# Kernel optimization log

Hardware: AMD Instinct MI355X
Metric: run time of the kernel (lower is better)

## Reference

```python
import jax, jax.numpy as jnp
import numpy as np

D_MODEL = 1024
N_HEAD = 16


def setup_inputs() -> dict:
    key = jax.random.key(0)
    ks = jax.random.split(key, 11)
    B, S, D = 2, 2048, D_MODEL
    scale = 1.0 / np.sqrt(D)
    inp = {
        "query_tensor": jax.random.normal(ks[0], (B, S, D), jnp.float32),
        "key_tensor": jax.random.normal(ks[1], (B, S, D), jnp.float32),
        "value_tensor": jax.random.normal(ks[2], (B, S, D), jnp.float32),
        "w_q": jax.random.normal(ks[3], (D, D), jnp.float32) * scale,
        "b_q": jnp.zeros((D,), jnp.float32),
        "w_k": jax.random.normal(ks[4], (D, D), jnp.float32) * scale,
        "b_k": jnp.zeros((D,), jnp.float32),
        "w_v": jax.random.normal(ks[5], (D, D), jnp.float32) * scale,
        "b_v": jnp.zeros((D,), jnp.float32),
        "w_out": jax.random.normal(ks[6], (D, D), jnp.float32) * scale,
        "b_out": jnp.zeros((D,), jnp.float32),
    }
    return inp


def _split_heads(x, n_head):
    b, s, d = x.shape
    return x.reshape(b, s, n_head, d // n_head).transpose(0, 2, 1, 3)  # [b,h,s,dk]


def reference(query_tensor, key_tensor, value_tensor, w_q, b_q, w_k, b_k, w_v, b_v, w_out, b_out):
    # torch Linear: y = x @ W.T + b
    q = query_tensor @ w_q.T + b_q
    k = key_tensor @ w_k.T + b_k
    v = value_tensor @ w_v.T + b_v
    q = _split_heads(q, N_HEAD)
    k = _split_heads(k, N_HEAD)
    v = _split_heads(v, N_HEAD)
    d_k = k.shape[-1]
    scores = jnp.einsum("bhqd,bhkd->bhqk", q, k) / jnp.sqrt(jnp.float32(d_k))
    attn = jax.nn.softmax(scores, axis=-1)
    ctx = jnp.einsum("bhqk,bhkd->bhqd", attn, v)
    b, h, s, dk = ctx.shape
    ctx = ctx.transpose(0, 2, 1, 3).reshape(b, s, h * dk)
    return ctx @ w_out.T + b_out
```

## Files before the change

### kernel.cpp

```cpp
#include <hip/hip_runtime.h>
#include <hip/hip_bf16.h>

using ushort = unsigned short;

typedef __attribute__((ext_vector_type(8))) short bf16x8;
typedef __attribute__((ext_vector_type(4))) float f32x4;
typedef __attribute__((ext_vector_type(16))) float f32x16;
typedef __attribute__((ext_vector_type(4))) unsigned short u16x4;

#define DEVINL __device__ __forceinline__


static constexpr size_t XQ_O = 0;
static constexpr size_t WQ_O = 12582912;
static constexpr size_t WO_O = 15728640;
static constexpr size_t QB_O = 16777216;
static constexpr size_t KB_O = 20971520;
static constexpr size_t VT_O = 25165824;
static constexpr size_t CTX_O = 0;

DEVINL ushort f2bf(float f) {
  unsigned u = __builtin_bit_cast(unsigned, f);
  u += 0x7fffu + ((u >> 16) & 1u);
  return (ushort)(u >> 16);
}

DEVINL void gld16(const ushort* g, ushort* lds) {
  __builtin_amdgcn_global_load_lds(
      (const __attribute__((address_space(1))) void*)g,
      (__attribute__((address_space(3))) void*)lds, 16, 0, 0);
}

__global__ __launch_bounds__(256) void cvt_all(
    const float* __restrict__ xq, const float* __restrict__ xk, const float* __restrict__ xv,
    const float* __restrict__ wq, const float* __restrict__ wk, const float* __restrict__ wv,
    const float* __restrict__ wo, ushort* __restrict__ ws)
{
  int e = (blockIdx.x * 256 + threadIdx.x) * 8;
  const float* s;
  if      (e < 4194304)  s = xq + e;
  else if (e < 8388608)  s = xk + (e - 4194304);
  else if (e < 12582912) s = xv + (e - 8388608);
  else if (e < 13631488) s = wq + (e - 12582912);
  else if (e < 14680064) s = wk + (e - 13631488);
  else if (e < 15728640) s = wv + (e - 14680064);
  else                   s = wo + (e - 15728640);
  float4 a = *(const float4*)s;
  float4 b = *(const float4*)(s + 4);
  union { u16x4 v; ushort u[4]; } r0, r1;
  r0.u[0] = f2bf(a.x); r0.u[1] = f2bf(a.y); r0.u[2] = f2bf(a.z); r0.u[3] = f2bf(a.w);
  r1.u[0] = f2bf(b.x); r1.u[1] = f2bf(b.y); r1.u[2] = f2bf(b.z); r1.u[3] = f2bf(b.w);
  *(u16x4*)(ws + e) = r0.v;
  *(u16x4*)(ws + e + 4) = r1.v;
}

DEVINL void gemm_core(const ushort* __restrict__ A, const ushort* __restrict__ Bw,
                      const float* __restrict__ bias, void* __restrict__ Cout,
                      float scale, int omode, int row0, int col0)
{
  constexpr int K = 1024;
  __shared__ ushort As[128 * 64];
  __shared__ ushort Bs[128 * 64];
  const int t = threadIdx.x;
  const int l = t & 63;
  const int w = t >> 6;
  const int wr = w >> 1, wc = w & 1;

  const int srow = t >> 3;
  const int scol8 = (t & 7) * 8;
  const int swz_half = ((((t & 7) * 16) ^ ((srow & 7) << 4)) >> 1);

  const ushort* Ap = A + (size_t)(row0 + srow) * K + scol8;
  const ushort* Bp = Bw + (size_t)(col0 + srow) * K + scol8;

  bf16x8 areg[4], breg[4];
  auto loadstage = [&](int k0) {
#pragma unroll
    for (int i = 0; i < 4; ++i) {
      areg[i] = *(const bf16x8*)(Ap + (size_t)(i * 32) * K + k0);
      breg[i] = *(const bf16x8*)(Bp + (size_t)(i * 32) * K + k0);
    }
  };

  f32x4 acc[4][4];
#pragma unroll
  for (int i = 0; i < 4; ++i)
#pragma unroll
    for (int j = 0; j < 4; ++j) acc[i][j] = (f32x4){0.f, 0.f, 0.f, 0.f};

  loadstage(0);
#pragma unroll 1
  for (int kt = 0; kt < K / 64; ++kt) {
    __syncthreads();
#pragma unroll
    for (int i = 0; i < 4; ++i) {
      *(bf16x8*)&As[(srow + i * 32) * 64 + swz_half] = areg[i];
      *(bf16x8*)&Bs[(srow + i * 32) * 64 + swz_half] = breg[i];
    }
    if (kt + 1 < K / 64) loadstage((kt + 1) * 64);
    __syncthreads();
#pragma unroll
    for (int ks = 0; ks < 2; ++ks) {
      bf16x8 af[4], bfr[4];
#pragma unroll
      for (int mi = 0; mi < 4; ++mi) {
        int r = wr * 64 + mi * 16 + (l & 15);
        int cb = ((ks << 6) | ((l >> 4) << 4)) ^ ((r & 7) << 4);
        af[mi] = *(const bf16x8*)&As[r * 64 + (cb >> 1)];
      }
#pragma unroll
      for (int nj = 0; nj < 4; ++nj) {
        int r = wc * 64 + nj * 16 + (l & 15);
        int cb = ((ks << 6) | ((l >> 4) << 4)) ^ ((r & 7) << 4);
        bfr[nj] = *(const bf16x8*)&Bs[r * 64 + (cb >> 1)];
      }
#pragma unroll
      for (int mi = 0; mi < 4; ++mi)
#pragma unroll
        for (int nj = 0; nj < 4; ++nj)
          acc[mi][nj] = __builtin_amdgcn_mfma_f32_16x16x32_bf16(af[mi], bfr[nj], acc[mi][nj], 0, 0, 0);
    }
  }

  const int cl = l & 15;
#pragma unroll
  for (int mi = 0; mi < 4; ++mi) {
#pragma unroll
    for (int nj = 0; nj < 4; ++nj) {
      int n = col0 + wc * 64 + nj * 16 + cl;
      float bv = bias[n];
      int mbase = row0 + wr * 64 + mi * 16 + (l >> 4) * 4;
      if (omode == 1) {
        float* Of = (float*)Cout;
#pragma unroll
        for (int ri = 0; ri < 4; ++ri)
          Of[(size_t)(mbase + ri) * 1024 + n] = (acc[mi][nj][ri] + bv) * scale;
      } else if (omode == 0) {
        ushort* Ob = (ushort*)Cout;
        int h = n >> 6, d = n & 63;
#pragma unroll
        for (int ri = 0; ri < 4; ++ri) {
          int m = mbase + ri;
          int b = m >> 11, s = m & 2047;
          Ob[(size_t)((b * 16 + h) * 2048 + s) * 64 + d] = f2bf((acc[mi][nj][ri] + bv) * scale);
        }
      } else {
        ushort* Ob = (ushort*)Cout;
        int h = n >> 6, d = n & 63;
        int b = mbase >> 11, s = mbase & 2047;
        union { u16x4 v; ushort u[4]; } pk;
#pragma unroll
        for (int ri = 0; ri < 4; ++ri) pk.u[ri] = f2bf((acc[mi][nj][ri] + bv) * scale);
        *(u16x4*)&Ob[(size_t)((b * 16 + h) * 64 + d) * 2048 + s] = pk.v;
      }
    }
  }
}

__global__ __launch_bounds__(256, 2) void gemm_qkv(
    const ushort* __restrict__ ws_c, ushort* __restrict__ ws_m,
    const float* __restrict__ bq, const float* __restrict__ bk, const float* __restrict__ bv)
{
  const int z = blockIdx.z;
  const ushort* A = ws_c + XQ_O + (size_t)z * 4194304;
  const ushort* W = ws_c + WQ_O + (size_t)z * 1048576;
  const float* bias = (z == 0) ? bq : ((z == 1) ? bk : bv);
  ushort* dst = ws_m + QB_O + (size_t)z * 4194304;
  float scale = (z == 0) ? (0.125f * 1.4426950408889634f) : 1.0f;
  int omode = (z == 2) ? 2 : 0;
  gemm_core(A, W, bias, dst, scale, omode, blockIdx.y * 128, blockIdx.x * 128);
}

__global__ __launch_bounds__(256, 2) void gemm_out(
    const ushort* __restrict__ ctx, const ushort* __restrict__ wo,
    const float* __restrict__ bo, float* __restrict__ out)
{
  gemm_core(ctx, wo, bo, out, 1.0f, 1, blockIdx.y * 128, blockIdx.x * 128);
}

__global__ __launch_bounds__(512, 4) void attn8(
    const ushort* __restrict__ Qb, const ushort* __restrict__ Kb,
    const ushort* __restrict__ Vtb, ushort* __restrict__ Ctx)
{
  __shared__ ushort smem[32768];

  const int t = threadIdx.x, l = t & 63, w = t >> 6;
  const int wq4 = w & 3, half = w >> 2;
  const int hi2 = l >> 5, q = l & 31;
  const int bh = blockIdx.y, qt = blockIdx.x;
  const int kvb = half * 1024;
  const ushort* Qp = Qb + ((size_t)bh * 2048 + qt * 128 + wq4 * 32) * 64;
  const ushort* Kp = Kb + (size_t)bh * 2048 * 64;
  const ushort* Vp = Vtb + (size_t)bh * 64 * 2048;

  ushort* Ksh = smem + half * 8192;
  ushort* Vsh = smem + 16384 + half * 8192;

  bf16x8 qf[4];
#pragma unroll
  for (int ks = 0; ks < 4; ++ks)
    qf[ks] = *(const bf16x8*)(Qp + q * 64 + ks * 16 + hi2 * 8);

  auto stageKV = [&](int pp, int kv0) {
#pragma unroll
    for (int i = 0; i < 2; ++i) {
      int R = (i * 4 + wq4) * 8 + (l >> 3);
      int g = l & 7;
      int sR = (R & ~12) | ((R & 4) << 1) | ((R & 8) >> 1);
      gld16(Kp + (size_t)(kv0 + sR) * 64 + (g ^ (R & 7)) * 8,
            Ksh + pp * 4096 + (i * 4 + wq4) * 512);
      gld16(Vp + (size_t)R * 2048 + kv0 + (g ^ (R & 7)) * 8,
            Vsh + pp * 4096 + (i * 4 + wq4) * 512);
    }
  };

  f32x16 acc0, acc1;
#pragma unroll
  for (int i = 0; i < 16; ++i) { acc0[i] = 0.f; acc1[i] = 0.f; }
  f32x16 Zv;
#pragma unroll
  for (int i = 0; i < 16; ++i) Zv[i] = 0.f;
  float lrun = 0.f;

  const int rsw = (q & 7) << 4;

  stageKV(0, kvb);
  __syncthreads();

#pragma unroll 1
  for (int kt = 0; kt < 16; ++kt) {
    const int p = kt & 1;
    const ushort* Kl = Ksh + p * 4096;
    const ushort* Vl = Vsh + p * 4096;

    f32x16 scA, scB;
    __builtin_amdgcn_s_setprio(1);
    {
      bf16x8 kf = *(const bf16x8*)&Kl[q * 64 + (((hi2 * 16)) ^ rsw) / 2];
      scA = __builtin_amdgcn_mfma_f32_32x32x16_bf16(kf, qf[0], Zv, 0, 0, 0);
#pragma unroll
      for (int ks = 1; ks < 4; ++ks) {
        bf16x8 k2 = *(const bf16x8*)&Kl[q * 64 + (((ks * 32 + hi2 * 16) ^ rsw) >> 1)];
        scA = __builtin_amdgcn_mfma_f32_32x32x16_bf16(k2, qf[ks], scA, 0, 0, 0);
      }
      const int r1 = (32 + q) * 64;
      bf16x8 kg = *(const bf16x8*)&Kl[r1 + (((hi2 * 16)) ^ rsw) / 2];
      scB = __builtin_amdgcn_mfma_f32_32x32x16_bf16(kg, qf[0], Zv, 0, 0, 0);
#pragma unroll
      for (int ks = 1; ks < 4; ++ks) {
        bf16x8 k2 = *(const bf16x8*)&Kl[r1 + (((ks * 32 + hi2 * 16) ^ rsw) >> 1)];
        scB = __builtin_amdgcn_mfma_f32_32x32x16_bf16(k2, qf[ks], scB, 0, 0, 0);
      }
    }
    __builtin_amdgcn_s_setprio(0);

    if (kt + 1 < 16) stageKV(p ^ 1, kvb + (kt + 1) * 64);

#pragma unroll
    for (int c = 0; c < 2; ++c) {
      f32x16& sc = (c == 0) ? scA : scB;
      float s0 = 0.f, s1 = 0.f, s2 = 0.f, s3 = 0.f;
#pragma unroll
      for (int i = 0; i < 4; ++i) {
        float e0 = __builtin_amdgcn_exp2f(sc[i]);      sc[i] = e0;      s0 += e0;
        float e1 = __builtin_amdgcn_exp2f(sc[4 + i]);  sc[4 + i] = e1;  s1 += e1;
        float e2 = __builtin_amdgcn_exp2f(sc[8 + i]);  sc[8 + i] = e2;  s2 += e2;
        float e3 = __builtin_amdgcn_exp2f(sc[12 + i]); sc[12 + i] = e3; s3 += e3;
      }
      lrun += (s0 + s1) + (s2 + s3);

      union PU { bf16x8 v; unsigned u[4]; } pA, pB;
#pragma unroll
      for (int i = 0; i < 4; ++i) {
        asm("v_cvt_pk_bf16_f32 %0, %1, %2" : "=v"(pA.u[i]) : "v"(sc[2 * i]), "v"(sc[2 * i + 1]));
        asm("v_cvt_pk_bf16_f32 %0, %1, %2" : "=v"(pB.u[i]) : "v"(sc[8 + 2 * i]), "v"(sc[9 + 2 * i]));
      }

      __builtin_amdgcn_s_setprio(1);
#pragma unroll
      for (int db = 0; db < 2; ++db) {
        const int d = db * 32 + q;
        bf16x8 va = *(const bf16x8*)&Vl[d * 64 + (((c * 64 + hi2 * 16) ^ rsw) >> 1)];
        bf16x8 vb = *(const bf16x8*)&Vl[d * 64 + (((c * 64 + 32 + hi2 * 16) ^ rsw) >> 1)];
        if (db == 0) {
          acc0 = __builtin_amdgcn_mfma_f32_32x32x16_bf16(va, pA.v, acc0, 0, 0, 0);
          acc0 = __builtin_amdgcn_mfma_f32_32x32x16_bf16(vb, pB.v, acc0, 0, 0, 0);
        } else {
          acc1 = __builtin_amdgcn_mfma_f32_32x32x16_bf16(va, pA.v, acc1, 0, 0, 0);
          acc1 = __builtin_amdgcn_mfma_f32_32x32x16_bf16(vb, pB.v, acc1, 0, 0, 0);
        }
      }
      __builtin_amdgcn_s_setprio(0);
    }
    __syncthreads();
  }

  float lsum = lrun + __shfl_xor(lrun, 32);
  float* Lf = (float*)smem;

  if (l < 32) Lf[half * 128 + wq4 * 32 + q] = lsum;
  __syncthreads();
  const float inv = 1.0f / (Lf[wq4 * 32 + q] + Lf[128 + wq4 * 32 + q]);
  __syncthreads();

  if (half == 1) {
    float* base = Lf + (wq4 * 32 + q) * 64;
#pragma unroll
    for (int db = 0; db < 2; ++db)
#pragma unroll
      for (int g = 0; g < 4; ++g) {
        float4 v;
        if (db == 0) v = (float4){acc0[g * 4], acc0[g * 4 + 1], acc0[g * 4 + 2], acc0[g * 4 + 3]};
        else         v = (float4){acc1[g * 4], acc1[g * 4 + 1], acc1[g * 4 + 2], acc1[g * 4 + 3]};
        *(float4*)(base + db * 32 + g * 8 + hi2 * 4) = v;
      }
  }
  __syncthreads();

  if (half == 0) {
    float* base = Lf + (wq4 * 32 + q) * 64;
#pragma unroll
    for (int db = 0; db < 2; ++db)
#pragma unroll
      for (int g = 0; g < 4; ++g) {
        float* p = base + db * 32 + g * 8 + hi2 * 4;
        float4 pv = *(float4*)p;
        float4 o;
        if (db == 0) o = (float4){(acc0[g * 4] + pv.x) * inv, (acc0[g * 4 + 1] + pv.y) * inv,
                                  (acc0[g * 4 + 2] + pv.z) * inv, (acc0[g * 4 + 3] + pv.w) * inv};
        else         o = (float4){(acc1[g * 4] + pv.x) * inv, (acc1[g * 4 + 1] + pv.y) * inv,
                                  (acc1[g * 4 + 2] + pv.z) * inv, (acc1[g * 4 + 3] + pv.w) * inv};
        *(float4*)p = o;
      }
  }
  __syncthreads();

  {
    const int b = bh >> 4, h = bh & 15;
    const int d0 = (l & 7) * 8;
#pragma unroll
    for (int rr = 0; rr < 2; ++rr) {
      int row = w * 16 + rr * 8 + (l >> 3);
      float4 f0 = *(const float4*)(Lf + row * 64 + d0);
      float4 f1 = *(const float4*)(Lf + row * 64 + d0 + 4);
      union { u16x4 v; ushort u[4]; } o0, o1;
      o0.u[0] = f2bf(f0.x); o0.u[1] = f2bf(f0.y); o0.u[2] = f2bf(f0.z); o0.u[3] = f2bf(f0.w);
      o1.u[0] = f2bf(f1.x); o1.u[1] = f2bf(f1.y); o1.u[2] = f2bf(f1.z); o1.u[3] = f2bf(f1.w);
      ushort* dst = Ctx + ((size_t)b * 2048 + qt * 128 + row) * 1024 + h * 64 + d0;
      *(u16x4*)dst = o0.v;
      *(u16x4*)(dst + 4) = o1.v;
    }
  }
}

extern "C" void kernel_launch(void* const* d_in, const int* in_sizes, int n_in,
                              void* d_out, int out_size, void* d_ws, size_t ws_size,
                              hipStream_t stream) {
  const float* xq = (const float*)d_in[0];
  const float* xk = (const float*)d_in[1];
  const float* xv = (const float*)d_in[2];
  const float* wq = (const float*)d_in[3];
  const float* bq = (const float*)d_in[4];
  const float* wk = (const float*)d_in[5];
  const float* bk = (const float*)d_in[6];
  const float* wv = (const float*)d_in[7];
  const float* bv = (const float*)d_in[8];
  const float* wo = (const float*)d_in[9];
  const float* bo = (const float*)d_in[10];
  ushort* ws = (ushort*)d_ws;

  cvt_all<<<8192, 256, 0, stream>>>(xq, xk, xv, wq, wk, wv, wo, ws);
  gemm_qkv<<<dim3(8, 32, 3), 256, 0, stream>>>(ws, ws, bq, bk, bv);
  attn8<<<dim3(16, 32), 512, 0, stream>>>(ws + QB_O, ws + KB_O, ws + VT_O, ws + CTX_O);
  gemm_out<<<dim3(8, 32), 256, 0, stream>>>(ws + CTX_O, ws + WO_O, bo, (float*)d_out);
}
```

Before: 116.9 us.

## Narrow output GEMM tile, remap attention blocks, swizzle merge LDS buffer

The output projection GEMM is templated on N-tile width and now uses 128x64 tiles, doubling its grid to 512 blocks so more CUs on the MI355X are busy. The attention kernel remaps block indices so that concurrently scheduled blocks share heads, which should improve L2 reuse of K/V. The fp32 LDS merge buffer is XOR-swizzled to cut bank conflicts during the two-half reduction and bf16 writeout. The narrower tile lowers per-block arithmetic intensity for the output GEMM.

New measurement: 114.4 us. 2.1% less time.

```diff
diff --git a/kernel.cpp b/kernel.cpp
--- a/kernel.cpp
+++ b/kernel.cpp
@@ -54,13 +54,16 @@
   *(u16x4*)(ws + e + 4) = r1.v;
 }
 
+template<int BN>
 DEVINL void gemm_core(const ushort* __restrict__ A, const ushort* __restrict__ Bw,
                       const float* __restrict__ bias, void* __restrict__ Cout,
                       float scale, int omode, int row0, int col0)
 {
   constexpr int K = 1024;
+  constexpr int BI = BN / 32;
+  constexpr int NJ = BN / 32;
   __shared__ ushort As[128 * 64];
-  __shared__ ushort Bs[128 * 64];
+  __shared__ ushort Bs[BN * 64];
   const int t = threadIdx.x;
   const int l = t & 63;
   const int w = t >> 6;
@@ -73,35 +76,37 @@
   const ushort* Ap = A + (size_t)(row0 + srow) * K + scol8;
   const ushort* Bp = Bw + (size_t)(col0 + srow) * K + scol8;
 
-  bf16x8 areg[4], breg[4];
+  bf16x8 areg[4], breg[BI];
   auto loadstage = [&](int k0) {
 #pragma unroll
-    for (int i = 0; i < 4; ++i) {
+    for (int i = 0; i < 4; ++i)
       areg[i] = *(const bf16x8*)(Ap + (size_t)(i * 32) * K + k0);
+#pragma unroll
+    for (int i = 0; i < BI; ++i)
       breg[i] = *(const bf16x8*)(Bp + (size_t)(i * 32) * K + k0);
-    }
   };
 
-  f32x4 acc[4][4];
+  f32x4 acc[4][NJ];
 #pragma unroll
   for (int i = 0; i < 4; ++i)
 #pragma unroll
-    for (int j = 0; j < 4; ++j) acc[i][j] = (f32x4){0.f, 0.f, 0.f, 0.f};
+    for (int j = 0; j < NJ; ++j) acc[i][j] = (f32x4){0.f, 0.f, 0.f, 0.f};
 
   loadstage(0);
 #pragma unroll 1
   for (int kt = 0; kt < K / 64; ++kt) {
     __syncthreads();
 #pragma unroll
-    for (int i = 0; i < 4; ++i) {
+    for (int i = 0; i < 4; ++i)
       *(bf16x8*)&As[(srow + i * 32) * 64 + swz_half] = areg[i];
+#pragma unroll
+    for (int i = 0; i < BI; ++i)
       *(bf16x8*)&Bs[(srow + i * 32) * 64 + swz_half] = breg[i];
-    }
     if (kt + 1 < K / 64) loadstage((kt + 1) * 64);
     __syncthreads();
 #pragma unroll
     for (int ks = 0; ks < 2; ++ks) {
-      bf16x8 af[4], bfr[4];
+      bf16x8 af[4], bfr[NJ];
 #pragma unroll
       for (int mi = 0; mi < 4; ++mi) {
         int r = wr * 64 + mi * 16 + (l & 15);
@@ -109,15 +114,15 @@
         af[mi] = *(const bf16x8*)&As[r * 64 + (cb >> 1)];
       }
 #pragma unroll
-      for (int nj = 0; nj < 4; ++nj) {
-        int r = wc * 64 + nj * 16 + (l & 15);
+      for (int nj = 0; nj < NJ; ++nj) {
+        int r = wc * (BN / 2) + nj * 16 + (l & 15);
         int cb = ((ks << 6) | ((l >> 4) << 4)) ^ ((r & 7) << 4);
         bfr[nj] = *(const bf16x8*)&Bs[r * 64 + (cb >> 1)];
       }
 #pragma unroll
       for (int mi = 0; mi < 4; ++mi)
 #pragma unroll
-        for (int nj = 0; nj < 4; ++nj)
+        for (int nj = 0; nj < NJ; ++nj)
           acc[mi][nj] = __builtin_amdgcn_mfma_f32_16x16x32_bf16(af[mi], bfr[nj], acc[mi][nj], 0, 0, 0);
     }
   }
@@ -126,8 +131,8 @@
 #pragma unroll
   for (int mi = 0; mi < 4; ++mi) {
 #pragma unroll
-    for (int nj = 0; nj < 4; ++nj) {
-      int n = col0 + wc * 64 + nj * 16 + cl;
+    for (int nj = 0; nj < NJ; ++nj) {
+      int n = col0 + wc * (BN / 2) + nj * 16 + cl;
       float bv = bias[n];
       int mbase = row0 + wr * 64 + mi * 16 + (l >> 4) * 4;
       if (omode == 1) {
@@ -168,14 +173,14 @@
   ushort* dst = ws_m + QB_O + (size_t)z * 4194304;
   float scale = (z == 0) ? (0.125f * 1.4426950408889634f) : 1.0f;
   int omode = (z == 2) ? 2 : 0;
-  gemm_core(A, W, bias, dst, scale, omode, blockIdx.y * 128, blockIdx.x * 128);
+  gemm_core<128>(A, W, bias, dst, scale, omode, blockIdx.y * 128, blockIdx.x * 128);
 }
 
 __global__ __launch_bounds__(256, 2) void gemm_out(
     const ushort* __restrict__ ctx, const ushort* __restrict__ wo,
     const float* __restrict__ bo, float* __restrict__ out)
 {
-  gemm_core(ctx, wo, bo, out, 1.0f, 1, blockIdx.y * 128, blockIdx.x * 128);
+  gemm_core<64>(ctx, wo, bo, out, 1.0f, 1, blockIdx.y * 128, blockIdx.x * 64);
 }
 
 __global__ __launch_bounds__(512, 4) void attn8(
@@ -187,7 +192,12 @@
   const int t = threadIdx.x, l = t & 63, w = t >> 6;
   const int wq4 = w & 3, half = w >> 2;
   const int hi2 = l >> 5, q = l & 31;
-  const int bh = blockIdx.y, qt = blockIdx.x;
+
+  const int hw = blockIdx.y * 16 + blockIdx.x;
+  const int j = hw >> 3;
+  const int bh = (hw & 7) + 8 * (j >> 4);
+  const int qt = j & 15;
+
   const int kvb = half * 1024;
   const ushort* Qp = Qb + ((size_t)bh * 2048 + qt * 128 + wq4 * 32) * 64;
   const ushort* Kp = Kb + (size_t)bh * 2048 * 64;
@@ -303,8 +313,12 @@
   const float inv = 1.0f / (Lf[wq4 * 32 + q] + Lf[128 + wq4 * 32 + q]);
   __syncthreads();
 
+  auto mrg = [&](int row, int G) -> float* {
+    return Lf + row * 64 + ((G ^ (row & 15)) << 2);
+  };
+
   if (half == 1) {
-    float* base = Lf + (wq4 * 32 + q) * 64;
+    const int row = wq4 * 32 + q;
 #pragma unroll
     for (int db = 0; db < 2; ++db)
 #pragma unroll
@@ -312,18 +326,18 @@
         float4 v;
         if (db == 0) v = (float4){acc0[g * 4], acc0[g * 4 + 1], acc0[g * 4 + 2], acc0[g * 4 + 3]};
         else         v = (float4){acc1[g * 4], acc1[g * 4 + 1], acc1[g * 4 + 2], acc1[g * 4 + 3]};
-        *(float4*)(base + db * 32 + g * 8 + hi2 * 4) = v;
+        *(float4*)mrg(row, db * 8 + g * 2 + hi2) = v;
       }
   }
   __syncthreads();
 
   if (half == 0) {
-    float* base = Lf + (wq4 * 32 + q) * 64;
+    const int row = wq4 * 32 + q;
 #pragma unroll
     for (int db = 0; db < 2; ++db)
 #pragma unroll
       for (int g = 0; g < 4; ++g) {
-        float* p = base + db * 32 + g * 8 + hi2 * 4;
+        float* p = mrg(row, db * 8 + g * 2 + hi2);
         float4 pv = *(float4*)p;
         float4 o;
         if (db == 0) o = (float4){(acc0[g * 4] + pv.x) * inv, (acc0[g * 4 + 1] + pv.y) * inv,
@@ -341,8 +355,8 @@
 #pragma unroll
     for (int rr = 0; rr < 2; ++rr) {
       int row = w * 16 + rr * 8 + (l >> 3);
-      float4 f0 = *(const float4*)(Lf + row * 64 + d0);
-      float4 f1 = *(const float4*)(Lf + row * 64 + d0 + 4);
+      float4 f0 = *(const float4*)mrg(row, (l & 7) * 2);
+      float4 f1 = *(const float4*)mrg(row, (l & 7) * 2 + 1);
       union { u16x4 v; ushort u[4]; } o0, o1;
       o0.u[0] = f2bf(f0.x); o0.u[1] = f2bf(f0.y); o0.u[2] = f2bf(f0.z); o0.u[3] = f2bf(f0.w);
       o1.u[0] = f2bf(f1.x); o1.u[1] = f2bf(f1.y); o1.u[2] = f2bf(f1.z); o1.u[3] = f2bf(f1.w);
@@ -372,5 +386,5 @@
   cvt_all<<<8192, 256, 0, stream>>>(xq, xk, xv, wq, wk, wv, wo, ws);
   gemm_qkv<<<dim3(8, 32, 3), 256, 0, stream>>>(ws, ws, bq, bk, bv);
   attn8<<<dim3(16, 32), 512, 0, stream>>>(ws + QB_O, ws + KB_O, ws + VT_O, ws + CTX_O);
-  gemm_out<<<dim3(8, 32), 256, 0, stream>>>(ws + CTX_O, ws + WO_O, bo, (float*)d_out);
-}
+  gemm_out<<<dim3(16, 32), 256, 0, stream>>>(ws + CTX_O, ws + WO_O, bo, (float*)d_out);
+}
```
